# Optimization experiments

Measured on AMD Instinct MI355X. Metric: run time of the kernel, lower is better.

Reference implementation:

```python
import jax, jax.numpy as jnp
import numpy as np

N_NODES = 100000
N_EDGES = 1600000
IN_CH, HID1, HID2, HID3, OUT_CH = 128, 64, 64, 256, 64


def gcn_conv(x, W, b, src, dst, n_nodes):
    """PyG GCNConv: linear transform, add self-loops, symmetric-normalized aggregation."""
    h = x @ W  # [N, d_out]
    # degree at target nodes, counting the self-loop (+1)
    deg = jnp.zeros((n_nodes,), dtype=h.dtype).at[dst].add(1.0) + 1.0
    dinv = jax.lax.rsqrt(deg)  # deg >= 1, safe
    norm = dinv[src] * dinv[dst]  # [E]
    # scatter-add normalized messages from src to dst
    agg = jnp.zeros_like(h).at[dst].add(h[src] * norm[:, None])
    # self-loop contribution: norm_ii = dinv[i]^2
    agg = agg + h * (dinv * dinv)[:, None]
    return agg + b


def setup_inputs() -> dict:
    key = jax.random.key(0)
    ks = jax.random.split(key, 8)
    x = jax.random.normal(ks[0], (N_NODES, IN_CH), dtype=jnp.float32)
    edge_index = jax.random.randint(ks[1], (2, N_EDGES), 0, N_NODES, dtype=jnp.int64)
    def glorot(k, fan_in, fan_out):
        s = jnp.sqrt(6.0 / (fan_in + fan_out)).astype(jnp.float32)
        return jax.random.uniform(k, (fan_in, fan_out), jnp.float32, -s, s)
    return {
        "x": x,
        "edge_index": edge_index,
        "W1": glorot(ks[2], IN_CH, HID1), "b1": jnp.zeros((HID1,), jnp.float32),
        "W2": glorot(ks[3], HID1, HID2), "b2": jnp.zeros((HID2,), jnp.float32),
        "W3": glorot(ks[4], HID2, HID3), "b3": jnp.zeros((HID3,), jnp.float32),
        "W4": glorot(ks[5], HID3, OUT_CH), "b4": jnp.zeros((OUT_CH,), jnp.float32),
    }


def reference(x, edge_index, W1, b1, W2, b2, W3, b3, W4, b4):
    src, dst = edge_index[0], edge_index[1]
    n = x.shape[0]
    h = jax.nn.relu(gcn_conv(x, W1, b1, src, dst, n))
    h = jax.nn.relu(gcn_conv(h, W2, b2, src, dst, n))
    h = h @ W3 + b3  # hidden Linear (no activation, per original forward)
    h = h @ W4 + b4  # output Linear
    return jax.nn.log_softmax(h, axis=-1)
```

## Files before the change

### kernel.cpp

```cpp
#include <hip/hip_runtime.h>
#include <hip/hip_bf16.h>
#include <math.h>

#define NNODES 100000
#define NEDGES 1600000
#define NB 782
#define PB 256
#define EPB 6250
#define SCAN_N (NB * PB)
#define CAP 4608

typedef __bf16 bf16x8 __attribute__((ext_vector_type(8)));
typedef float f32x4 __attribute__((ext_vector_type(4)));
typedef float f32x8 __attribute__((ext_vector_type(8)));

static __device__ inline unsigned short f2bf(float f) {
    __hip_bfloat16 h = __float2bfloat16(f);
    return *reinterpret_cast<unsigned short*>(&h);
}


__global__ __launch_bounds__(256) void hist_kernel(const int* __restrict__ dst,
                                                   int* __restrict__ histg) {
    __shared__ int h[NB];
    int tid = threadIdx.x, blk = blockIdx.x;
    for (int b = tid; b < NB; b += 256) h[b] = 0;
    __syncthreads();
    int base = blk * EPB;
    for (int i = base + tid; i < base + EPB; i += 256)
        atomicAdd(&h[dst[i] >> 7], 1);
    __syncthreads();
    for (int b = tid; b < NB; b += 256) histg[b * PB + blk] = h[b];
}


__global__ __launch_bounds__(256) void scan1_kernel(const int* __restrict__ cnt,
                                                    int* __restrict__ off,
                                                    int* __restrict__ bsum, int n) {
    __shared__ int tmp[256];
    int tid = threadIdx.x;
    int t4 = blockIdx.x * 1024 + tid * 4;
    int v0 = (t4 + 0 < n) ? cnt[t4 + 0] : 0;
    int v1 = (t4 + 1 < n) ? cnt[t4 + 1] : 0;
    int v2 = (t4 + 2 < n) ? cnt[t4 + 2] : 0;
    int v3 = (t4 + 3 < n) ? cnt[t4 + 3] : 0;
    int ssum = v0 + v1 + v2 + v3;
    tmp[tid] = ssum;
    __syncthreads();
    for (int d = 1; d < 256; d <<= 1) {
        int x = (tid >= d) ? tmp[tid - d] : 0;
        __syncthreads();
        tmp[tid] += x;
        __syncthreads();
    }
    int run = tmp[tid] - ssum;
    if (t4 + 0 < n) off[t4 + 0] = run; run += v0;
    if (t4 + 1 < n) off[t4 + 1] = run; run += v1;
    if (t4 + 2 < n) off[t4 + 2] = run; run += v2;
    if (t4 + 3 < n) off[t4 + 3] = run;
    if (tid == 255) bsum[blockIdx.x] = tmp[255];
}

__global__ __launch_bounds__(256) void scan2_kernel(const int* __restrict__ bsum,
                                                    int* __restrict__ bsum_ex, int nb) {
    __shared__ int tmp[256];
    int tid = threadIdx.x;
    int v = (tid < nb) ? bsum[tid] : 0;
    tmp[tid] = v;
    __syncthreads();
    for (int d = 1; d < 256; d <<= 1) {
        int x = (tid >= d) ? tmp[tid - d] : 0;
        __syncthreads();
        tmp[tid] += x;
        __syncthreads();
    }
    bsum_ex[tid] = tmp[tid] - v;
}

__global__ __launch_bounds__(256) void scan3t_kernel(const int* __restrict__ part_scan,
                                                     const int* __restrict__ bsum_ex,
                                                     int* __restrict__ gbaseT, int n) {
    int i = blockIdx.x * 256 + threadIdx.x;
    if (i < n) {
        int v = part_scan[i] + bsum_ex[i >> 10];
        int b = i >> 8, blk = i & 255;
        gbaseT[blk * NB + b] = v;
    }
}


__global__ __launch_bounds__(256) void part_kernel(const int* __restrict__ src,
                                                   const int* __restrict__ dst,
                                                   const int* __restrict__ gbaseT,
                                                   unsigned int* __restrict__ part) {
    __shared__ int gcol[NB];
    __shared__ int cur[NB];
    int tid = threadIdx.x, blk = blockIdx.x;
    for (int b = tid; b < NB; b += 256) {
        gcol[b] = gbaseT[blk * NB + b];
        cur[b] = 0;
    }
    __syncthreads();
    int base = blk * EPB;
    for (int i = base + tid; i < base + EPB; i += 256) {
        int s = src[i], d = dst[i];
        int bkt = d >> 7;
        int r = atomicAdd(&cur[bkt], 1);
        part[gcol[bkt] + r] = ((unsigned int)(d & 127) << 17) | (unsigned int)s;
    }
}


__global__ __launch_bounds__(256) void csr_kernel(const unsigned int* __restrict__ part,
                                                  const int* __restrict__ gbaseT,
                                                  int* __restrict__ csr,
                                                  int* __restrict__ cnt_g,
                                                  int* __restrict__ off_g,
                                                  float* __restrict__ dinv_g, int n) {
    __shared__ unsigned int stage[CAP];
    __shared__ int hist2[128];
    __shared__ int sc[128];
    __shared__ int excl[128];
    __shared__ int cur2[128];
    int tid = threadIdx.x, b = blockIdx.x;
    int S = gbaseT[b];
    int T = (b == NB - 1) ? NEDGES : gbaseT[b + 1];
    int len = T - S;
    bool fit = (len <= CAP);
    if (tid < 128) { hist2[tid] = 0; cur2[tid] = 0; }
    __syncthreads();
    for (int i = tid; i < len; i += 256) {
        unsigned int p = part[S + i];
        if (fit) stage[i] = p;
        atomicAdd(&hist2[p >> 17], 1);
    }
    __syncthreads();
    if (tid < 128) sc[tid] = hist2[tid];
    __syncthreads();
    for (int d = 1; d < 128; d <<= 1) {
        int x = 0;
        if (tid < 128 && tid >= d) x = sc[tid - d];
        __syncthreads();
        if (tid < 128) sc[tid] += x;
        __syncthreads();
    }
    if (tid < 128) {
        int c = hist2[tid];
        int ex = sc[tid] - c;
        excl[tid] = ex;
        int node = b * 128 + tid;
        if (node < n) {
            cnt_g[node] = c;
            off_g[node] = S + ex;
            dinv_g[node] = rsqrtf((float)c + 1.0f);
        }
    }
    __syncthreads();
    for (int i = tid; i < len; i += 256) {
        unsigned int p = fit ? stage[i] : part[S + i];
        int dl = p >> 17;
        int s = (int)(p & 0x1FFFFu);
        int r = atomicAdd(&cur2[dl], 1);
        csr[S + excl[dl] + r] = s;
    }
}


static __device__ inline int packidx64(int k, int ch) {
    int s = k >> 5, r5 = k & 31, q = r5 >> 3, ii = r5 & 7;
    int t = ch >> 4, lo = ch & 15;
    int lane = q * 16 + lo;
    return ((t * 2 + s) * 64 + lane) * 8 + ii;
}

__global__ __launch_bounds__(256) void prep_kernel(const float* __restrict__ W1,
                                                   const float* __restrict__ W2,
                                                   const float* __restrict__ W3,
                                                   const float* __restrict__ W4,
                                                   const float* __restrict__ b3,
                                                   const float* __restrict__ b4,
                                                   unsigned short* __restrict__ Wp1,
                                                   unsigned short* __restrict__ Wp2,
                                                   unsigned short* __restrict__ Wp34,
                                                   float* __restrict__ b34,
                                                   unsigned short* __restrict__ hp) {
    int blk = blockIdx.x, tid = threadIdx.x;
    if (blk < 32) {
        int idx = blk * 256 + tid;
        int i = idx & 7, rest = idx >> 3;
        int lane = rest & 63; rest >>= 6;
        int s = rest % 4, t = rest / 4;
        int k = s * 32 + (lane >> 4) * 8 + i;
        int ch = t * 16 + (lane & 15);
        Wp1[idx] = f2bf(W1[k * 64 + ch]);
    } else if (blk < 48) {
        int idx = (blk - 32) * 256 + tid;
        int i = idx & 7, rest = idx >> 3;
        int lane = rest & 63; rest >>= 6;
        int s = rest % 2, t = rest / 2;
        int k = s * 32 + (lane >> 4) * 8 + i;
        int ch = t * 16 + (lane & 15);
        Wp2[idx] = f2bf(W2[k * 64 + ch]);
    } else if (blk == 48) {
        if (tid < 64) hp[(size_t)NNODES * 64 + tid] = 0;
    } else if (blk < 65) {
        int i = (blk - 49) * 4 + (tid >> 6);
        int j = tid & 63;
        float a = 0.f;
        for (int k = 0; k < 256; ++k) a = fmaf(W3[i * 256 + k], W4[k * 64 + j], a);
        Wp34[packidx64(i, j)] = f2bf(a);
    } else {
        if (tid < 64) {
            int j = tid;
            float a = b4[j];
            for (int k = 0; k < 256; ++k) a = fmaf(b3[k], W4[k * 64 + j], a);
            b34[j] = a;
        }
    }
}


template <int K, bool LSM, bool F32IN>
__global__ __launch_bounds__(256) void gemm_mfma_kernel(const unsigned short* __restrict__ Xb,
                                                        const float* __restrict__ Xf,
                                                        const unsigned short* __restrict__ Wp,
                                                        const float* __restrict__ bias,
                                                        const float* __restrict__ dinv,
                                                        unsigned short* __restrict__ outb,
                                                        float* __restrict__ outf, int n) {
    constexpr int S = K / 32;
    int w = threadIdx.x >> 6, lane = threadIdx.x & 63;
    int q = lane >> 4, lo = lane & 15;
    int base = blockIdx.x * 64 + w * 16;
    int nodeA = base + lo;
    int na = nodeA < n ? nodeA : 0;

    f32x4 acc[4] = {};
#pragma unroll
    for (int s = 0; s < S; ++s) {
        bf16x8 a;
        if (F32IN) {
            const float* xr = Xf + (size_t)na * K + q * 8 + s * 32;
            float4 u = *(const float4*)(xr);
            float4 v = *(const float4*)(xr + 4);
            a[0] = (__bf16)u.x; a[1] = (__bf16)u.y; a[2] = (__bf16)u.z; a[3] = (__bf16)u.w;
            a[4] = (__bf16)v.x; a[5] = (__bf16)v.y; a[6] = (__bf16)v.z; a[7] = (__bf16)v.w;
        } else {
            a = *(const bf16x8*)(Xb + (size_t)na * K + q * 8 + s * 32);
        }
#pragma unroll
        for (int t = 0; t < 4; ++t) {
            bf16x8 b = *(const bf16x8*)(Wp + ((size_t)(t * S + s) * 64 + lane) * 8);
            acc[t] = __builtin_amdgcn_mfma_f32_16x16x32_bf16(a, b, acc[t], 0, 0, 0);
        }
    }

    if (!LSM) {
#pragma unroll
        for (int r = 0; r < 4; ++r) {
            int node = base + q * 4 + r;
            if (node < n) {
                float di = dinv[node];
#pragma unroll
                for (int t = 0; t < 4; ++t)
                    outb[(size_t)node * 64 + t * 16 + lo] = f2bf(acc[t][r] * di);
            }
        }
    } else {
#pragma unroll
        for (int r = 0; r < 4; ++r) {
            int node = base + q * 4 + r;
            float v0 = acc[0][r] + bias[0 * 16 + lo];
            float v1 = acc[1][r] + bias[1 * 16 + lo];
            float v2 = acc[2][r] + bias[2 * 16 + lo];
            float v3 = acc[3][r] + bias[3 * 16 + lo];
            float mx = fmaxf(fmaxf(v0, v1), fmaxf(v2, v3));
            for (int d = 1; d < 16; d <<= 1) mx = fmaxf(mx, __shfl_xor(mx, d));
            float sm = __expf(v0 - mx) + __expf(v1 - mx) + __expf(v2 - mx) + __expf(v3 - mx);
            for (int d = 1; d < 16; d <<= 1) sm += __shfl_xor(sm, d);
            float lse = mx + __logf(sm);
            if (node < n) {
                outf[(size_t)node * 64 + 0 * 16 + lo] = v0 - lse;
                outf[(size_t)node * 64 + 1 * 16 + lo] = v1 - lse;
                outf[(size_t)node * 64 + 2 * 16 + lo] = v2 - lse;
                outf[(size_t)node * 64 + 3 * 16 + lo] = v3 - lse;
            }
        }
    }
}


__global__ __launch_bounds__(256) void aggregate_kernel(const unsigned short* __restrict__ hp,
                                                        const int* __restrict__ csr,
                                                        const int* __restrict__ off,
                                                        const int* __restrict__ cnt,
                                                        const float* __restrict__ dinv,
                                                        const float* __restrict__ bias,
                                                        unsigned short* __restrict__ out, int n) {
    int wid = (blockIdx.x * 256 + threadIdx.x) >> 6;
    int lane = threadIdx.x & 63;
    if (wid >= n) return;
    int g = lane >> 3;
    int cb = (lane & 7) * 16;

    int s = off[wid];
    int c = cnt[wid];

    int ob = n << 7;
    if (lane < c) ob = csr[s + lane] << 7;
    else if (lane == c) ob = wid << 7;

    int m = (c <= 63) ? c + 1 : 64;
    int steps = (m + 7) >> 3;

    const char* hb = (const char*)hp;
    f32x8 acc0 = {}, acc1 = {};
    int it = 0;
    for (; it + 2 <= steps; it += 2) {
        int oa = __shfl(ob, it * 8 + g);
        int oc = __shfl(ob, it * 8 + 8 + g);
        bf16x8 va = *(const bf16x8*)(hb + oa + cb);
        bf16x8 vb = *(const bf16x8*)(hb + oc + cb);
        acc0 += __builtin_convertvector(va, f32x8);
        acc1 += __builtin_convertvector(vb, f32x8);
    }
    if (it < steps) {
        int oa = __shfl(ob, it * 8 + g);
        bf16x8 va = *(const bf16x8*)(hb + oa + cb);
        acc0 += __builtin_convertvector(va, f32x8);
    }

    if (c > 63) {
        if (g == 0) {
            bf16x8 v = *(const bf16x8*)(hb + ((size_t)wid << 7) + cb);
            acc1 += __builtin_convertvector(v, f32x8);
        }
        for (int jj = 64 + g; jj < c; jj += 8) {
            int srcn = csr[s + jj];
            bf16x8 v = *(const bf16x8*)(hb + ((size_t)srcn << 7) + cb);
            acc0 += __builtin_convertvector(v, f32x8);
        }
    }

    acc0 += acc1;

#pragma unroll
    for (int d = 8; d < 64; d <<= 1) {
        f32x8 t;
#pragma unroll
        for (int j = 0; j < 8; ++j) t[j] = __shfl_xor(acc0[j], d);
        acc0 += t;
    }

    if (lane < 8) {
        int c8 = lane * 8;
        float di = dinv[wid];
        float4 bv0 = *(const float4*)(bias + c8);
        float4 bv1 = *(const float4*)(bias + c8 + 4);
        float bb[8] = {bv0.x, bv0.y, bv0.z, bv0.w, bv1.x, bv1.y, bv1.z, bv1.w};
        unsigned short ov[8];
#pragma unroll
        for (int j = 0; j < 8; ++j)
            ov[j] = f2bf(fmaxf(fmaf(acc0[j], di, bb[j]), 0.f));
        *(ushort4*)(out + (size_t)wid * 64 + c8) = make_ushort4(ov[0], ov[1], ov[2], ov[3]);
        *(ushort4*)(out + (size_t)wid * 64 + c8 + 4) = make_ushort4(ov[4], ov[5], ov[6], ov[7]);
    }
}


extern "C" void kernel_launch(void* const* d_in, const int* in_sizes, int n_in,
                              void* d_out, int out_size, void* d_ws, size_t ws_size,
                              hipStream_t stream) {
    const float* x  = (const float*)d_in[0];
    const int*   ei = (const int*)d_in[1];
    const float* W1 = (const float*)d_in[2];
    const float* b1 = (const float*)d_in[3];
    const float* W2 = (const float*)d_in[4];
    const float* b2 = (const float*)d_in[5];
    const float* W3 = (const float*)d_in[6];
    const float* b3 = (const float*)d_in[7];
    const float* W4 = (const float*)d_in[8];
    const float* b4 = (const float*)d_in[9];
    float* outp = (float*)d_out;

    const int N = NNODES;
    const int E = NEDGES;
    const int* srcp = ei;
    const int* dstp = ei + E;

    char* w = (char*)d_ws;
    size_t o = 0;
    auto alloc = [&](size_t bytes) { size_t r = o; o = (o + bytes + 255) & ~(size_t)255; return r; };
    size_t cnt_off   = alloc((size_t)N * 4);
    size_t off_off   = alloc((size_t)N * 4);
    size_t dinv_off  = alloc((size_t)N * 4);
    size_t histg_off = alloc((size_t)SCAN_N * 4);
    size_t gscan_off = alloc((size_t)SCAN_N * 4);
    size_t gbT_off   = alloc((size_t)SCAN_N * 4);
    size_t bs_off    = alloc(256 * 4);
    size_t bse_off   = alloc(256 * 4);
    size_t part_off  = alloc((size_t)E * 4);
    size_t csr_off   = alloc((size_t)E * 4);
    size_t hp_off    = alloc((size_t)(N + 1) * 64 * 2);
    size_t abf_off   = alloc((size_t)N * 64 * 2);
    size_t wp1_off   = alloc(128 * 64 * 2);
    size_t wp2_off   = alloc(64 * 64 * 2);
    size_t wp34_off  = alloc(64 * 64 * 2);
    size_t b34_off   = alloc(64 * 4);

    int*            cnt   = (int*)(w + cnt_off);
    int*            off   = (int*)(w + off_off);
    float*          dinv  = (float*)(w + dinv_off);
    int*            histg = (int*)(w + histg_off);
    int*            gscan = (int*)(w + gscan_off);
    int*            gbT   = (int*)(w + gbT_off);
    int*            bs    = (int*)(w + bs_off);
    int*            bse   = (int*)(w + bse_off);
    unsigned int*   part  = (unsigned int*)(w + part_off);
    int*            csr   = (int*)(w + csr_off);
    unsigned short* hp    = (unsigned short*)(w + hp_off);
    unsigned short* abf   = (unsigned short*)(w + abf_off);
    unsigned short* Wp1   = (unsigned short*)(w + wp1_off);
    unsigned short* Wp2   = (unsigned short*)(w + wp2_off);
    unsigned short* Wp34  = (unsigned short*)(w + wp34_off);
    float*          b34   = (float*)(w + b34_off);

    const int sb = (SCAN_N + 1023) / 1024;
    const int s3b = (SCAN_N + 255) / 256;

    hist_kernel<<<PB, 256, 0, stream>>>(dstp, histg);
    scan1_kernel<<<sb, 256, 0, stream>>>(histg, gscan, bs, SCAN_N);
    scan2_kernel<<<1, 256, 0, stream>>>(bs, bse, sb);
    scan3t_kernel<<<s3b, 256, 0, stream>>>(gscan, bse, gbT, SCAN_N);
    part_kernel<<<PB, 256, 0, stream>>>(srcp, dstp, gbT, part);
    csr_kernel<<<NB, 256, 0, stream>>>(part, gbT, csr, cnt, off, dinv, N);

    prep_kernel<<<66, 256, 0, stream>>>(W1, W2, W3, W4, b3, b4, Wp1, Wp2, Wp34, b34, hp);

    const int gb = (N + 63) / 64;
    const int ab = (N + 3) / 4;

    gemm_mfma_kernel<128, false, true><<<gb, 256, 0, stream>>>(nullptr, x, Wp1, nullptr, dinv, hp, nullptr, N);
    aggregate_kernel<<<ab, 256, 0, stream>>>(hp, csr, off, cnt, dinv, b1, abf, N);
    gemm_mfma_kernel<64, false, false><<<gb, 256, 0, stream>>>(abf, nullptr, Wp2, nullptr, dinv, hp, nullptr, N);
    aggregate_kernel<<<ab, 256, 0, stream>>>(hp, csr, off, cnt, dinv, b2, abf, N);
    gemm_mfma_kernel<64, true, false><<<gb, 256, 0, stream>>>(abf, nullptr, Wp34, b34, nullptr, nullptr, outp, N);
}
```

Measured before the change: 289.1 us.

## Stage partitioned edges in LDS before global scatter; rewrite aggregate accumulation

The partition kernel now does a local prefix scan over the per-block bucket counts, places edges into a shared-memory sorted buffer together with their global destinations, and then writes them out in bucket order. Consecutive threads therefore store to mostly contiguous addresses instead of scattering across 782 buckets. The scan3t kernel also writes a transposed count array to feed that scan, which costs an extra 200K-int array and about 50KB of LDS per block. Separately, the aggregate kernel switches from byte offsets and vector converts to element indexing with scalar float accumulation arrays, which is mostly a cosmetic codegen change.

```diff
diff --git a/kernel.cpp b/kernel.cpp
--- a/kernel.cpp
+++ b/kernel.cpp
@@ -12,11 +12,15 @@
 
 typedef __bf16 bf16x8 __attribute__((ext_vector_type(8)));
 typedef float f32x4 __attribute__((ext_vector_type(4)));
-typedef float f32x8 __attribute__((ext_vector_type(8)));
 
 static __device__ inline unsigned short f2bf(float f) {
     __hip_bfloat16 h = __float2bfloat16(f);
     return *reinterpret_cast<unsigned short*>(&h);
+}
+
+static __device__ inline float bf2f(unsigned short u) {
+    unsigned int x = ((unsigned int)u) << 16;
+    return __builtin_bit_cast(float, x);
 }
 
 
@@ -79,12 +83,15 @@
 
 __global__ __launch_bounds__(256) void scan3t_kernel(const int* __restrict__ part_scan,
                                                      const int* __restrict__ bsum_ex,
-                                                     int* __restrict__ gbaseT, int n) {
+                                                     const int* __restrict__ histg,
+                                                     int* __restrict__ gbaseT,
+                                                     int* __restrict__ cntT, int n) {
     int i = blockIdx.x * 256 + threadIdx.x;
     if (i < n) {
         int v = part_scan[i] + bsum_ex[i >> 10];
         int b = i >> 8, blk = i & 255;
         gbaseT[blk * NB + b] = v;
+        cntT[blk * NB + b] = histg[i];
     }
 }
 
@@ -92,22 +99,53 @@
 __global__ __launch_bounds__(256) void part_kernel(const int* __restrict__ src,
                                                    const int* __restrict__ dst,
                                                    const int* __restrict__ gbaseT,
+                                                   const int* __restrict__ cntT,
                                                    unsigned int* __restrict__ part) {
+    __shared__ unsigned int sorted[EPB];
+    __shared__ int gaddr[EPB];
     __shared__ int gcol[NB];
+    __shared__ int base_l[NB];
     __shared__ int cur[NB];
+    __shared__ int tmp[256];
     int tid = threadIdx.x, blk = blockIdx.x;
     for (int b = tid; b < NB; b += 256) {
         gcol[b] = gbaseT[blk * NB + b];
+        base_l[b] = cntT[blk * NB + b];
         cur[b] = 0;
     }
+    __syncthreads();
+    int t4 = tid * 4;
+    int v0 = (t4 + 0 < NB) ? base_l[t4 + 0] : 0;
+    int v1 = (t4 + 1 < NB) ? base_l[t4 + 1] : 0;
+    int v2 = (t4 + 2 < NB) ? base_l[t4 + 2] : 0;
+    int v3 = (t4 + 3 < NB) ? base_l[t4 + 3] : 0;
+    int ssum = v0 + v1 + v2 + v3;
+    tmp[tid] = ssum;
+    __syncthreads();
+    for (int d = 1; d < 256; d <<= 1) {
+        int x = (tid >= d) ? tmp[tid - d] : 0;
+        __syncthreads();
+        tmp[tid] += x;
+        __syncthreads();
+    }
+    int run = tmp[tid] - ssum;
+    if (t4 + 0 < NB) base_l[t4 + 0] = run; run += v0;
+    if (t4 + 1 < NB) base_l[t4 + 1] = run; run += v1;
+    if (t4 + 2 < NB) base_l[t4 + 2] = run; run += v2;
+    if (t4 + 3 < NB) base_l[t4 + 3] = run;
     __syncthreads();
     int base = blk * EPB;
     for (int i = base + tid; i < base + EPB; i += 256) {
         int s = src[i], d = dst[i];
         int bkt = d >> 7;
         int r = atomicAdd(&cur[bkt], 1);
-        part[gcol[bkt] + r] = ((unsigned int)(d & 127) << 17) | (unsigned int)s;
-    }
+        int pos = base_l[bkt] + r;
+        sorted[pos] = ((unsigned int)(d & 127) << 17) | (unsigned int)s;
+        gaddr[pos] = gcol[bkt] + r;
+    }
+    __syncthreads();
+    for (int i = tid; i < EPB; i += 256)
+        part[gaddr[i]] = sorted[i];
 }
 
 
@@ -301,59 +339,58 @@
     int lane = threadIdx.x & 63;
     if (wid >= n) return;
     int g = lane >> 3;
-    int cb = (lane & 7) * 16;
+    int c8 = (lane & 7) * 8;
 
     int s = off[wid];
     int c = cnt[wid];
 
-    int ob = n << 7;
-    if (lane < c) ob = csr[s + lane] << 7;
-    else if (lane == c) ob = wid << 7;
+    int idx = n;
+    if (lane < c) idx = csr[s + lane];
+    else if (lane == c) idx = wid;
 
     int m = (c <= 63) ? c + 1 : 64;
     int steps = (m + 7) >> 3;
 
-    const char* hb = (const char*)hp;
-    f32x8 acc0 = {}, acc1 = {};
+    float acc0[8] = {}, acc1[8] = {};
     int it = 0;
     for (; it + 2 <= steps; it += 2) {
-        int oa = __shfl(ob, it * 8 + g);
-        int oc = __shfl(ob, it * 8 + 8 + g);
-        bf16x8 va = *(const bf16x8*)(hb + oa + cb);
-        bf16x8 vb = *(const bf16x8*)(hb + oc + cb);
-        acc0 += __builtin_convertvector(va, f32x8);
-        acc1 += __builtin_convertvector(vb, f32x8);
+        int sa = __shfl(idx, it * 8 + g);
+        int sb = __shfl(idx, it * 8 + 8 + g);
+        bf16x8 va = *(const bf16x8*)(hp + (size_t)sa * 64 + c8);
+        bf16x8 vb = *(const bf16x8*)(hp + (size_t)sb * 64 + c8);
+#pragma unroll
+        for (int j = 0; j < 8; ++j) { acc0[j] += (float)va[j]; acc1[j] += (float)vb[j]; }
     }
     if (it < steps) {
-        int oa = __shfl(ob, it * 8 + g);
-        bf16x8 va = *(const bf16x8*)(hb + oa + cb);
-        acc0 += __builtin_convertvector(va, f32x8);
+        int sa = __shfl(idx, it * 8 + g);
+        bf16x8 va = *(const bf16x8*)(hp + (size_t)sa * 64 + c8);
+#pragma unroll
+        for (int j = 0; j < 8; ++j) acc0[j] += (float)va[j];
     }
 
     if (c > 63) {
         if (g == 0) {
-            bf16x8 v = *(const bf16x8*)(hb + ((size_t)wid << 7) + cb);
-            acc1 += __builtin_convertvector(v, f32x8);
+            bf16x8 v = *(const bf16x8*)(hp + (size_t)wid * 64 + c8);
+#pragma unroll
+            for (int j = 0; j < 8; ++j) acc1[j] += (float)v[j];
         }
         for (int jj = 64 + g; jj < c; jj += 8) {
             int srcn = csr[s + jj];
-            bf16x8 v = *(const bf16x8*)(hb + ((size_t)srcn << 7) + cb);
-            acc0 += __builtin_convertvector(v, f32x8);
-        }
-    }
-
-    acc0 += acc1;
-
-#pragma unroll
-    for (int d = 8; d < 64; d <<= 1) {
-        f32x8 t;
-#pragma unroll
-        for (int j = 0; j < 8; ++j) t[j] = __shfl_xor(acc0[j], d);
-        acc0 += t;
-    }
+            bf16x8 v = *(const bf16x8*)(hp + (size_t)srcn * 64 + c8);
+#pragma unroll
+            for (int j = 0; j < 8; ++j) acc0[j] += (float)v[j];
+        }
+    }
+
+#pragma unroll
+    for (int j = 0; j < 8; ++j) acc0[j] += acc1[j];
+
+#pragma unroll
+    for (int d = 8; d < 64; d <<= 1)
+#pragma unroll
+        for (int j = 0; j < 8; ++j) acc0[j] += __shfl_xor(acc0[j], d);
 
     if (lane < 8) {
-        int c8 = lane * 8;
         float di = dinv[wid];
         float4 bv0 = *(const float4*)(bias + c8);
         float4 bv1 = *(const float4*)(bias + c8 + 4);
@@ -397,6 +434,7 @@
     size_t histg_off = alloc((size_t)SCAN_N * 4);
     size_t gscan_off = alloc((size_t)SCAN_N * 4);
     size_t gbT_off   = alloc((size_t)SCAN_N * 4);
+    size_t cntT_off  = alloc((size_t)SCAN_N * 4);
     size_t bs_off    = alloc(256 * 4);
     size_t bse_off   = alloc(256 * 4);
     size_t part_off  = alloc((size_t)E * 4);
@@ -414,6 +452,7 @@
     int*            histg = (int*)(w + histg_off);
     int*            gscan = (int*)(w + gscan_off);
     int*            gbT   = (int*)(w + gbT_off);
+    int*            cntT  = (int*)(w + cntT_off);
     int*            bs    = (int*)(w + bs_off);
     int*            bse   = (int*)(w + bse_off);
     unsigned int*   part  = (unsigned int*)(w + part_off);
@@ -431,8 +470,8 @@
     hist_kernel<<<PB, 256, 0, stream>>>(dstp, histg);
     scan1_kernel<<<sb, 256, 0, stream>>>(histg, gscan, bs, SCAN_N);
     scan2_kernel<<<1, 256, 0, stream>>>(bs, bse, sb);
-    scan3t_kernel<<<s3b, 256, 0, stream>>>(gscan, bse, gbT, SCAN_N);
-    part_kernel<<<PB, 256, 0, stream>>>(srcp, dstp, gbT, part);
+    scan3t_kernel<<<s3b, 256, 0, stream>>>(gscan, bse, histg, gbT, cntT, SCAN_N);
+    part_kernel<<<PB, 256, 0, stream>>>(srcp, dstp, gbT, cntT, part);
     csr_kernel<<<NB, 256, 0, stream>>>(part, gbT, csr, cnt, off, dinv, N);
 
     prep_kernel<<<66, 256, 0, stream>>>(W1, W2, W3, W4, b3, b4, Wp1, Wp2, Wp34, b34, hp);
```

After: 270.9 us. -6.3%, faster.
